# Optimization experiments

Measured on AMD Instinct MI355X. Metric: run time of the kernel, lower is better.

Reference implementation:

```python
import jax, jax.numpy as jnp
import numpy as np

B, H, S, D = 2, 16, 2048, 128

def setup_inputs() -> dict:
    key = jax.random.key(0)
    k1, k2, k3, k4 = jax.random.split(key, 4)
    queries = jax.random.normal(k1, (B, H, S, D), dtype=jnp.float32)
    keys = jax.random.normal(k2, (B, H, S, D), dtype=jnp.float32)
    values = jax.random.normal(k3, (B, H, S, D), dtype=jnp.float32)
    mask = jax.random.randint(k4, (B, 1, S, S), 0, 2).astype(jnp.int32)
    return {"queries": queries, "keys": keys, "values": values, "d_k": D, "mask": mask}

def reference(queries, keys, values, d_k, mask):
    # scores: [B, H, S, S]
    scale = 1.0 / jnp.sqrt(jnp.float32(d_k))
    scores = jnp.einsum('bhqd,bhkd->bhqk', queries, keys) * scale
    if mask is not None:
        scores = scores + (-1e9) * mask.astype(scores.dtype)
    weights = jax.nn.softmax(scores, axis=-1)
    out = jnp.einsum('bhqk,bhkd->bhqd', weights, values)
    return out
```

## Files before the change

kernel.cpp:

```cpp
#include <hip/hip_runtime.h>
#include <hip/hip_bf16.h>

#define BB 2
#define HH 16
#define SS 2048
#define DD 128
#define QBLK 128
#define KVBLK 64
#define NT (SS / KVBLK)
#define TILE_ELEMS (KVBLK * DD)

typedef __bf16 bf16x8 __attribute__((ext_vector_type(8)));
typedef float  f32x16 __attribute__((ext_vector_type(16)));

#define EXP2(x) __builtin_amdgcn_exp2f(x)
#define M2FIX 20.0f

__global__ __launch_bounds__(256)
void kimg_prep(const float* __restrict__ K, __bf16* __restrict__ Kd)
{
    #pragma unroll
    for (int i = 0; i < 4; ++i) {
        const int g   = blockIdx.x * 1024 + i * 256 + threadIdx.x;
        const int row = g >> 4;
        const int u   = (g & 15) ^ (row & 15);
        const float* src = K + (size_t)row * 128 + u * 8;
        float4 f0 = *(const float4*)src;
        float4 f1 = *(const float4*)(src + 4);
        bf16x8 h;
        h[0]=(__bf16)f0.x; h[1]=(__bf16)f0.y; h[2]=(__bf16)f0.z; h[3]=(__bf16)f0.w;
        h[4]=(__bf16)f1.x; h[5]=(__bf16)f1.y; h[6]=(__bf16)f1.z; h[7]=(__bf16)f1.w;
        *(bf16x8*)(Kd + (size_t)g * 8) = h;
    }
}

__global__ __launch_bounds__(256)
void vimg_prep(const float* __restrict__ V, __bf16* __restrict__ Vd)
{
    const int g    = blockIdx.x * 256 + threadIdx.x;
    const int tile = g >> 10;
    const int wu   = g & 1023;
    const int d    = wu >> 3;
    const int iu   = wu & 7;
    const int us   = iu ^ (d & 7);
    const int c    = us >> 1;
    const int hh   = us & 1;
    const float* src = V + ((size_t)tile * 64 + c * 16 + 4 * hh) * 128 + d;
    bf16x8 o;
    #pragma unroll
    for (int j = 0; j < 8; ++j) {
        const int roff = (j & 3) + 8 * (j >> 2);
        o[j] = (__bf16)src[(size_t)roff * 128];
    }
    *(bf16x8*)(Vd + (size_t)g * 8) = o;
}

__global__ __launch_bounds__(256)
void mprep(const int* __restrict__ M, unsigned* __restrict__ mb)
{
    const int wid  = blockIdx.x * 4 + (threadIdx.x >> 6);
    const int lane = threadIdx.x & 63;
    const int kb   = wid & 31;
    const int q    = (wid >> 5) & 2047;
    const int b    = wid >> 16;
    const int mi   = M[((size_t)b * 2048 + q) * 2048 + kb * 64 + lane];
    const unsigned long long bal = __ballot(mi != 0);
    if (lane == 0) {
        uint2 st; st.x = (unsigned)bal; st.y = (unsigned)(bal >> 32);
        *(uint2*)&mb[((size_t)b * 2048 + q) * 64 + kb * 2] = st;
    }
}

__device__ __forceinline__ void load_lds16(const __bf16* g, __bf16* l) {
    __builtin_amdgcn_global_load_lds(
        (const __attribute__((address_space(1))) void*)g,
        (__attribute__((address_space(3))) void*)l, 16, 0, 0);
}

#define WAIT_VM(N)                                                             \
    do {                                                                       \
        asm volatile("s_waitcnt vmcnt(" #N ")" ::: "memory");                  \
        __builtin_amdgcn_sched_barrier(0);                                     \
    } while (0)

#define BAR() __builtin_amdgcn_s_barrier()

#define ISSUE_LDS(BUF)                                                         \
    do {                                                                       \
        _Pragma("unroll")                                                      \
        for (int i = 0; i < 4; ++i)                                            \
            load_lds16(kgp + i * 512, SM + (BUF) * 8192 + w * 2048 + i * 512); \
        _Pragma("unroll")                                                      \
        for (int i = 0; i < 4; ++i)                                            \
            load_lds16(vgp + i * 512, SM + 16384 + (BUF) * 8192 + w * 2048 + i * 512); \
        kgp += TILE_ELEMS;                                                     \
        vgp += TILE_ELEMS;                                                     \
    } while (0)

#define ISSUE_M(MST)                                                           \
    do { MST = *(const uint2*)mp; mp += 2; } while (0)

#define COMPUTE_TILE(BUF, MST)                                                 \
    do {                                                                       \
        f32x16 s[2];                                                           \
        __builtin_amdgcn_s_setprio(1);                                         \
        _Pragma("unroll")                                                      \
        for (int ko = 0; ko < 2; ++ko) {                                       \
            s[ko] = (f32x16)0.0f;                                              \
            _Pragma("unroll")                                                  \
            for (int d0 = 0; d0 < 8; ++d0) {                                   \
                bf16x8 kf = *(const bf16x8*)(kp[d0] + (BUF) * 8192 + ko * 4096); \
                s[ko] = __builtin_amdgcn_mfma_f32_32x32x16_bf16(kf, qf[d0], s[ko], 0, 0, 0); \
            }                                                                  \
        }                                                                      \
        __builtin_amdgcn_s_setprio(0);                                         \
        float rs0 = 0.0f, rs1 = 0.0f;                                          \
        _Pragma("unroll")                                                      \
        for (int c = 0; c < 4; ++c) {                                          \
            const int ko = c >> 1, cc = c & 1;                                 \
            const unsigned wc = ((ko ? MST.y : MST.x) >> sh4) >> (16 * cc);    \
            bf16x8 pb;                                                         \
            _Pragma("unroll")                                                  \
            for (int r = 0; r < 8; ++r) {                                      \
                float p = EXP2(s[ko][cc * 8 + r] - M2FIX);                     \
                p = (wc & (1u << ((r & 3) + 8 * (r >> 2)))) ? 0.0f : p;        \
                if (c & 1) rs1 += p; else rs0 += p;                            \
                pb[r] = (__bf16)p;                                             \
            }                                                                  \
            __builtin_amdgcn_s_setprio(1);                                     \
            _Pragma("unroll")                                                  \
            for (int dd = 0; dd < 4; ++dd) {                                   \
                bf16x8 va = *(const bf16x8*)(vp[c] + (BUF) * 8192 + dd * 2048); \
                o[dd] = __builtin_amdgcn_mfma_f32_32x32x16_bf16(va, pb, o[dd], 0, 0, 0); \
            }                                                                  \
            __builtin_amdgcn_s_setprio(0);                                     \
        }                                                                      \
        l_i += rs0 + rs1;                                                      \
    } while (0)

#define HALF_ITER(BUF, MREG)                                                   \
    do {                                                                       \
        COMPUTE_TILE(BUF, MREG);                                               \
        BAR();                                                                 \
        ISSUE_LDS(BUF);                                                        \
        ISSUE_M(MREG);                                                         \
        WAIT_VM(9);                                                            \
        BAR();                                                                 \
    } while (0)

__global__ __launch_bounds__(256, 2)
void attn_fwd(const float* __restrict__ Q, const __bf16* __restrict__ Kimg,
              const __bf16* __restrict__ Vimg, const unsigned* __restrict__ MB,
              float* __restrict__ O)
{
    __shared__ __bf16 SM[4 * TILE_ELEMS];

    const int tid  = threadIdx.x;
    const int lane = tid & 63;
    const int ln31 = lane & 31;
    const int h    = lane >> 5;
    const int w    = tid >> 6;
    const int sh4  = 4 * h;

    const int bid = blockIdx.x;
    const int swz = (bid & 7) * 64 + (bid >> 3);
    const int qb  = swz & 15;
    const int bh  = swz >> 4;
    const int b   = bh >> 4;

    const float SC = 0.08838834764831845f * 1.4426950408889634f;

    const float* Qb = Q + (size_t)bh * SS * DD;
    float*       Ob = O + (size_t)bh * SS * DD;

    const int qrow = qb * QBLK + w * 32 + ln31;

    const __bf16*   kgp = Kimg + (size_t)bh * SS * DD + w * 2048 + lane * 8;
    const __bf16*   vgp = Vimg + (size_t)bh * SS * DD + w * 2048 + lane * 8;
    const unsigned* mp  = MB + ((size_t)b * 2048 + qrow) * 64;

    const int kkey = ln31 & 15;
    const int vkey = ln31 & 7;
    const __bf16* kp[8];
    #pragma unroll
    for (int j = 0; j < 8; ++j)
        kp[j] = SM + ln31 * 128 + (((j * 2 + h) ^ kkey) * 8);
    const __bf16* vp[4];
    #pragma unroll
    for (int j = 0; j < 4; ++j)
        vp[j] = SM + 16384 + ln31 * 64 + (((j * 2 + h) ^ vkey) * 8);

    bf16x8 qf[8];
    {
        const float* qr = Qb + (size_t)qrow * DD + 8 * h;
        #pragma unroll
        for (int d0 = 0; d0 < 8; ++d0) {
            float4 f0 = *(const float4*)(qr + d0 * 16);
            float4 f1 = *(const float4*)(qr + d0 * 16 + 4);
            bf16x8 a;
            a[0]=(__bf16)(f0.x*SC); a[1]=(__bf16)(f0.y*SC);
            a[2]=(__bf16)(f0.z*SC); a[3]=(__bf16)(f0.w*SC);
            a[4]=(__bf16)(f1.x*SC); a[5]=(__bf16)(f1.y*SC);
            a[6]=(__bf16)(f1.z*SC); a[7]=(__bf16)(f1.w*SC);
            qf[d0] = a;
        }
    }
    __builtin_amdgcn_sched_barrier(0);

    f32x16 o[4];
    #pragma unroll
    for (int i = 0; i < 4; ++i) o[i] = (f32x16)0.0f;
    float l_i = 0.0f;

    uint2 mA, mB2;

    ISSUE_LDS(0);
    ISSUE_M(mA);
    ISSUE_LDS(1);
    ISSUE_M(mB2);
    WAIT_VM(9);
    BAR();

    #pragma unroll 1
    for (int t = 0; t + 3 < NT; t += 2) {
        HALF_ITER(0, mA);
        HALF_ITER(1, mB2);
    }
    COMPUTE_TILE(0, mA);
    WAIT_VM(0);
    BAR();
    COMPUTE_TILE(1, mB2);

    l_i += __shfl_xor(l_i, 32);
    const float inv = (l_i > 0.0f) ? 1.0f / l_i : 0.0f;
    float* orow = Ob + (size_t)qrow * DD + 4 * h;
    #pragma unroll
    for (int dd = 0; dd < 4; ++dd) {
        #pragma unroll
        for (int rg = 0; rg < 4; ++rg) {
            float4 st;
            st.x = o[dd][rg*4+0] * inv; st.y = o[dd][rg*4+1] * inv;
            st.z = o[dd][rg*4+2] * inv; st.w = o[dd][rg*4+3] * inv;
            *(float4*)&orow[dd * 32 + rg * 8] = st;
        }
    }
}

extern "C" void kernel_launch(void* const* d_in, const int* in_sizes, int n_in,
                              void* d_out, int out_size, void* d_ws, size_t ws_size,
                              hipStream_t stream) {
    const float* Q = (const float*)d_in[0];
    const float* K = (const float*)d_in[1];
    const float* V = (const float*)d_in[2];
    const int*   M = (const int*)d_in[4];
    float*       O = (float*)d_out;

    const size_t NE = (size_t)BB * HH * SS * DD;
    __bf16*   Kimg = (__bf16*)d_ws;
    __bf16*   Vimg = Kimg + NE;
    unsigned* Mbit = (unsigned*)(Vimg + NE);

    kimg_prep<<<1024, 256, 0, stream>>>(K, Kimg);
    vimg_prep<<<4096, 256, 0, stream>>>(V, Vimg);
    mprep    <<<32768, 256, 0, stream>>>(M, Mbit);

    attn_fwd<<<BB * HH * (SS / QBLK), 256, 0, stream>>>(Q, Kimg, Vimg, Mbit, O);
}
```

Before: 126.2 us.

## Software-pipeline QK/softmax of next tile with PV of current tile

Restructures the attention main loop so that the QK^T MFMAs and exp/mask for tile t+1 are interleaved with the PV MFMAs for tile t. Probabilities are held in double-buffered register arrays, with a prologue and epilogue handling the first and last tiles. The V LDS image is re-swizzled at 4-element granularity, with matching changes to the prep kernel and pointer setup, which changes how LDS bank conflicts fall. The priority hints are removed and each step now waits on vmcnt(0), which adds register pressure and may expose load latency at the barrier.

```diff
diff --git a/kernel.cpp b/kernel.cpp
--- a/kernel.cpp
+++ b/kernel.cpp
@@ -11,6 +11,7 @@
 #define TILE_ELEMS (KVBLK * DD)
 
 typedef __bf16 bf16x8 __attribute__((ext_vector_type(8)));
+typedef __bf16 bf16x4 __attribute__((ext_vector_type(4)));
 typedef float  f32x16 __attribute__((ext_vector_type(16)));
 
 #define EXP2(x) __builtin_amdgcn_exp2f(x)
@@ -38,21 +39,21 @@
 void vimg_prep(const float* __restrict__ V, __bf16* __restrict__ Vd)
 {
     const int g    = blockIdx.x * 256 + threadIdx.x;
-    const int tile = g >> 10;
-    const int wu   = g & 1023;
-    const int d    = wu >> 3;
-    const int iu   = wu & 7;
-    const int us   = iu ^ (d & 7);
-    const int c    = us >> 1;
-    const int hh   = us & 1;
-    const float* src = V + ((size_t)tile * 64 + c * 16 + 4 * hh) * 128 + d;
-    bf16x8 o;
-    #pragma unroll
-    for (int j = 0; j < 8; ++j) {
-        const int roff = (j & 3) + 8 * (j >> 2);
-        o[j] = (__bf16)src[(size_t)roff * 128];
-    }
-    *(bf16x8*)(Vd + (size_t)g * 8) = o;
+    const int tile = g >> 11;
+    const int wu   = g & 2047;
+    const int d    = wu >> 4;
+    const int u    = wu & 15;
+    const int s    = u ^ (d & 15);
+    const int c    = s >> 2;
+    const int hh   = (s >> 1) & 1;
+    const int bb   = s & 1;
+    const float* src = V + ((size_t)tile * 64 + c * 16 + 4 * hh + 8 * bb) * 128 + d;
+    bf16x4 o;
+    o[0] = (__bf16)src[0];
+    o[1] = (__bf16)src[128];
+    o[2] = (__bf16)src[256];
+    o[3] = (__bf16)src[384];
+    *(bf16x4*)(Vd + (size_t)g * 4) = o;
 }
 
 __global__ __launch_bounds__(256)
@@ -89,63 +90,72 @@
     do {                                                                       \
         _Pragma("unroll")                                                      \
         for (int i = 0; i < 4; ++i)                                            \
-            load_lds16(kgp + i * 512, SM + (BUF) * 8192 + w * 2048 + i * 512); \
+            load_lds16(kgp + i * 512, SMEM + (BUF) * 8192 + w * 2048 + i * 512); \
         _Pragma("unroll")                                                      \
         for (int i = 0; i < 4; ++i)                                            \
-            load_lds16(vgp + i * 512, SM + 16384 + (BUF) * 8192 + w * 2048 + i * 512); \
+            load_lds16(vgp + i * 512, SMEM + 16384 + (BUF) * 8192 + w * 2048 + i * 512); \
         kgp += TILE_ELEMS;                                                     \
         vgp += TILE_ELEMS;                                                     \
     } while (0)
 
-#define ISSUE_M(MST)                                                           \
-    do { MST = *(const uint2*)mp; mp += 2; } while (0)
-
-#define COMPUTE_TILE(BUF, MST)                                                 \
-    do {                                                                       \
-        f32x16 s[2];                                                           \
-        __builtin_amdgcn_s_setprio(1);                                         \
-        _Pragma("unroll")                                                      \
-        for (int ko = 0; ko < 2; ++ko) {                                       \
-            s[ko] = (f32x16)0.0f;                                              \
-            _Pragma("unroll")                                                  \
-            for (int d0 = 0; d0 < 8; ++d0) {                                   \
-                bf16x8 kf = *(const bf16x8*)(kp[d0] + (BUF) * 8192 + ko * 4096); \
-                s[ko] = __builtin_amdgcn_mfma_f32_32x32x16_bf16(kf, qf[d0], s[ko], 0, 0, 0); \
-            }                                                                  \
-        }                                                                      \
-        __builtin_amdgcn_s_setprio(0);                                         \
-        float rs0 = 0.0f, rs1 = 0.0f;                                          \
+#define QK_TILE(BUF, S0, S1)                                                   \
+    do {                                                                       \
+        S0 = (f32x16)0.0f; S1 = (f32x16)0.0f;                                  \
+        _Pragma("unroll")                                                      \
+        for (int d0 = 0; d0 < 8; ++d0) {                                       \
+            bf16x8 kf0 = *(const bf16x8*)(kp[d0] + (BUF) * 8192);              \
+            bf16x8 kf1 = *(const bf16x8*)(kp[d0] + (BUF) * 8192 + 4096);       \
+            S0 = __builtin_amdgcn_mfma_f32_32x32x16_bf16(kf0, qf[d0], S0, 0, 0, 0); \
+            S1 = __builtin_amdgcn_mfma_f32_32x32x16_bf16(kf1, qf[d0], S1, 0, 0, 0); \
+        }                                                                      \
+    } while (0)
+
+#define SM_TILE(S0, S1, MREG, PB)                                              \
+    do {                                                                       \
+        const unsigned w0 = (MREG).x >> sh4;                                   \
+        const unsigned w1 = (MREG).y >> sh4;                                   \
+        float rs = 0.0f;                                                       \
         _Pragma("unroll")                                                      \
         for (int c = 0; c < 4; ++c) {                                          \
-            const int ko = c >> 1, cc = c & 1;                                 \
-            const unsigned wc = ((ko ? MST.y : MST.x) >> sh4) >> (16 * cc);    \
-            bf16x8 pb;                                                         \
+            const unsigned wc = ((c & 2) ? w1 : w0) >> (16 * (c & 1));         \
             _Pragma("unroll")                                                  \
             for (int r = 0; r < 8; ++r) {                                      \
-                float p = EXP2(s[ko][cc * 8 + r] - M2FIX);                     \
+                float p = EXP2((((c & 2) ? S1 : S0)[(c & 1) * 8 + r]) - M2FIX);\
                 p = (wc & (1u << ((r & 3) + 8 * (r >> 2)))) ? 0.0f : p;        \
-                if (c & 1) rs1 += p; else rs0 += p;                            \
-                pb[r] = (__bf16)p;                                             \
+                rs += p;                                                       \
+                (PB)[c][r] = (__bf16)p;                                        \
             }                                                                  \
-            __builtin_amdgcn_s_setprio(1);                                     \
+        }                                                                      \
+        l_i += rs;                                                             \
+    } while (0)
+
+#define PV_TILE(BUF, PB)                                                       \
+    do {                                                                       \
+        _Pragma("unroll")                                                      \
+        for (int c = 0; c < 4; ++c) {                                          \
             _Pragma("unroll")                                                  \
             for (int dd = 0; dd < 4; ++dd) {                                   \
-                bf16x8 va = *(const bf16x8*)(vp[c] + (BUF) * 8192 + dd * 2048); \
-                o[dd] = __builtin_amdgcn_mfma_f32_32x32x16_bf16(va, pb, o[dd], 0, 0, 0); \
+                bf16x4 lo = *(const bf16x4*)(vp[c * 2]     + (BUF) * 8192 + dd * 2048); \
+                bf16x4 hi = *(const bf16x4*)(vp[c * 2 + 1] + (BUF) * 8192 + dd * 2048); \
+                bf16x8 va = __builtin_shufflevector(lo, hi, 0, 1, 2, 3, 4, 5, 6, 7); \
+                o[dd] = __builtin_amdgcn_mfma_f32_32x32x16_bf16(va, (PB)[c], o[dd], 0, 0, 0); \
             }                                                                  \
-            __builtin_amdgcn_s_setprio(0);                                     \
-        }                                                                      \
-        l_i += rs0 + rs1;                                                      \
-    } while (0)
-
-#define HALF_ITER(BUF, MREG)                                                   \
-    do {                                                                       \
-        COMPUTE_TILE(BUF, MREG);                                               \
+        }                                                                      \
+    } while (0)
+
+#define BODY(BUFC, PB_USE, PB_FILL, MREG, DO_ISSUE)                            \
+    do {                                                                       \
+        WAIT_VM(0);                                                            \
         BAR();                                                                 \
-        ISSUE_LDS(BUF);                                                        \
-        ISSUE_M(MREG);                                                         \
-        WAIT_VM(9);                                                            \
+        f32x16 s0, s1;                                                         \
+        QK_TILE((BUFC) ^ 1, s0, s1);                                           \
+        SM_TILE(s0, s1, MREG, PB_FILL);                                        \
+        PV_TILE(BUFC, PB_USE);                                                 \
         BAR();                                                                 \
+        if (DO_ISSUE) {                                                        \
+            ISSUE_LDS(BUFC);                                                   \
+            MREG = *(const uint2*)mp; mp += 2;                                 \
+        }                                                                      \
     } while (0)
 
 __global__ __launch_bounds__(256, 2)
@@ -153,7 +163,7 @@
               const __bf16* __restrict__ Vimg, const unsigned* __restrict__ MB,
               float* __restrict__ O)
 {
-    __shared__ __bf16 SM[4 * TILE_ELEMS];
+    __shared__ __bf16 SMEM[4 * TILE_ELEMS];
 
     const int tid  = threadIdx.x;
     const int lane = tid & 63;
@@ -179,16 +189,17 @@
     const __bf16*   vgp = Vimg + (size_t)bh * SS * DD + w * 2048 + lane * 8;
     const unsigned* mp  = MB + ((size_t)b * 2048 + qrow) * 64;
 
-    const int kkey = ln31 & 15;
-    const int vkey = ln31 & 7;
+    const int key = ln31 & 15;
     const __bf16* kp[8];
     #pragma unroll
     for (int j = 0; j < 8; ++j)
-        kp[j] = SM + ln31 * 128 + (((j * 2 + h) ^ kkey) * 8);
-    const __bf16* vp[4];
-    #pragma unroll
-    for (int j = 0; j < 4; ++j)
-        vp[j] = SM + 16384 + ln31 * 64 + (((j * 2 + h) ^ vkey) * 8);
+        kp[j] = SMEM + ln31 * 128 + (((j * 2 + h) ^ key) * 8);
+    const __bf16* vp[8];
+    #pragma unroll
+    for (int u = 0; u < 8; ++u) {
+        const int c = u >> 1, bb = u & 1;
+        vp[u] = SMEM + 16384 + ln31 * 64 + (((c * 4 + 2 * h + bb) ^ key) * 4);
+    }
 
     bf16x8 qf[8];
     {
@@ -212,24 +223,29 @@
     for (int i = 0; i < 4; ++i) o[i] = (f32x16)0.0f;
     float l_i = 0.0f;
 
-    uint2 mA, mB2;
+    bf16x8 pbE[4], pbO[4];
+    uint2 mE, mO;
 
     ISSUE_LDS(0);
-    ISSUE_M(mA);
+    uint2 mPro = *(const uint2*)mp; mp += 2;
     ISSUE_LDS(1);
-    ISSUE_M(mB2);
-    WAIT_VM(9);
+    mE = *(const uint2*)mp; mp += 2;
+    mO = *(const uint2*)mp; mp += 2;
+    WAIT_VM(6);
     BAR();
+    {
+        f32x16 s0, s1;
+        QK_TILE(0, s0, s1);
+        SM_TILE(s0, s1, mPro, pbO);
+    }
 
     #pragma unroll 1
-    for (int t = 0; t + 3 < NT; t += 2) {
-        HALF_ITER(0, mA);
-        HALF_ITER(1, mB2);
-    }
-    COMPUTE_TILE(0, mA);
-    WAIT_VM(0);
-    BAR();
-    COMPUTE_TILE(1, mB2);
+    for (int t = 0; t < 30; t += 2) {
+        BODY(0, pbO, pbE, mE, 1);
+        BODY(1, pbE, pbO, mO, 1);
+    }
+    BODY(0, pbO, pbE, mE, 0);
+    PV_TILE(1, pbE);
 
     l_i += __shfl_xor(l_i, 32);
     const float inv = (l_i > 0.0f) ? 1.0f / l_i : 0.0f;
@@ -261,7 +277,7 @@
     unsigned* Mbit = (unsigned*)(Vimg + NE);
 
     kimg_prep<<<1024, 256, 0, stream>>>(K, Kimg);
-    vimg_prep<<<4096, 256, 0, stream>>>(V, Vimg);
+    vimg_prep<<<8192, 256, 0, stream>>>(V, Vimg);
     mprep    <<<32768, 256, 0, stream>>>(M, Mbit);
 
     attn_fwd<<<BB * HH * (SS / QBLK), 256, 0, stream>>>(Q, Kimg, Vimg, Mbit, O);
```

After: 130.2 us. +3.2%, slower.
